# Performance work log

Hardware: AMD Instinct MI355X
Metric: run time of the kernel (lower is better)

## Reference

```python
import jax, jax.numpy as jnp
import numpy as np

RES = 28      # input feature-map resolution
RES2 = 14     # ceil(RES/2) after downsample
NH = 8        # num_heads
KD = 16       # key_dim
D = 64        # attn_ratio * key_dim (per-head value dim)
DH = 512      # D * NH
N = RES * RES
N2 = RES2 * RES2


def _rel_idx():
    # Matches tf.meshgrid default 'xy' indexing in set_attention_bias_idxs.
    r = RES
    kp = np.stack(np.meshgrid(np.arange(r), np.arange(r), indexing='xy')).reshape(2, -1)
    qp = np.stack(np.meshgrid(np.arange(0, r, 2), np.arange(0, r, 2), indexing='xy')).reshape(2, -1)
    rel = np.abs(qp[:, :, None] - kp[:, None, :])
    return jnp.asarray(rel[0] * r + rel[1], dtype=jnp.int32)  # [N2, N]

REL_IDX = _rel_idx()


def _dw_stride2(x, w, b):
    # Depthwise 3x3 conv, stride 2, TF 'SAME' padding. w: [3,3,1,C]
    c = x.shape[-1]
    y = jax.lax.conv_general_dilated(
        x, w, window_strides=(2, 2), padding='SAME',
        dimension_numbers=('NHWC', 'HWIO', 'NHWC'), feature_group_count=c)
    return y + b


def setup_inputs() -> dict:
    key = jax.random.key(0)
    ks = jax.random.split(key, 10)
    f = jnp.float32
    C, OUT = 384, 768
    return {
        'x': jax.random.normal(ks[0], (64, RES, RES, C), f),
        'q_local_w': jax.random.normal(ks[1], (3, 3, 1, C), f) * 0.1,
        'q_local_b': jnp.zeros((C,), f),
        'q_proj_w': jax.random.normal(ks[2], (C, NH * KD), f) * 0.05,
        'q_proj_b': jnp.zeros((NH * KD,), f),
        'q_bn_s': jnp.ones((NH * KD,), f),
        'q_bn_b': jnp.zeros((NH * KD,), f),
        'k_w': jax.random.normal(ks[3], (C, NH * KD), f) * 0.05,
        'k_b': jnp.zeros((NH * KD,), f),
        'k_bn_s': jnp.ones((NH * KD,), f),
        'k_bn_b': jnp.zeros((NH * KD,), f),
        'v_w': jax.random.normal(ks[4], (C, DH), f) * 0.05,
        'v_b': jnp.zeros((DH,), f),
        'v_bn_s': jnp.ones((DH,), f),
        'v_bn_b': jnp.zeros((DH,), f),
        'vloc_w': jax.random.normal(ks[5], (3, 3, 1, DH), f) * 0.1,
        'vloc_b': jnp.zeros((DH,), f),
        'vloc_bn_s': jnp.ones((DH,), f),
        'vloc_bn_b': jnp.zeros((DH,), f),
        'proj_w': jax.random.normal(ks[6], (DH, OUT), f) * 0.05,
        'proj_b': jnp.zeros((OUT,), f),
        'proj_bn_s': jnp.ones((OUT,), f),
        'proj_bn_b': jnp.zeros((OUT,), f),
        'attn_bias': jax.random.normal(ks[7], (NH, N), f) * 0.1,
    }


def reference(x, q_local_w, q_local_b, q_proj_w, q_proj_b, q_bn_s, q_bn_b,
              k_w, k_b, k_bn_s, k_bn_b, v_w, v_b, v_bn_s, v_bn_b,
              vloc_w, vloc_b, vloc_bn_s, vloc_bn_b,
              proj_w, proj_b, proj_bn_s, proj_bn_b, attn_bias):
    B = x.shape[0]
    scale = KD ** -0.5
    # LGQuery: depthwise-conv local branch + 1x1 avg-pool (stride-2 subsample)
    q = _dw_stride2(x, q_local_w, q_local_b) + x[:, ::2, ::2, :]
    q = (q @ q_proj_w + q_proj_b) * q_bn_s + q_bn_b          # [B,14,14,128]
    k = (x @ k_w + k_b) * k_bn_s + k_bn_b                    # [B,28,28,128]
    v = (x @ v_w + v_b) * v_bn_s + v_bn_b                    # [B,28,28,512]
    v_local = _dw_stride2(v, vloc_w, vloc_b) * vloc_bn_s + vloc_bn_b  # [B,14,14,512]
    qh = q.reshape(B, N2, NH, KD).transpose(0, 2, 1, 3)      # [B,H,N2,KD]
    kh = k.reshape(B, N, NH, KD).transpose(0, 2, 3, 1)       # [B,H,KD,N]
    vh = v.reshape(B, N, NH, D).transpose(0, 2, 1, 3)        # [B,H,N,D]
    attn = (qh @ kh) * scale + attn_bias[:, REL_IDX]         # [B,H,N2,N]
    attn = jax.nn.softmax(attn, axis=-1)
    out = (attn @ vh).transpose(0, 2, 1, 3).reshape(B, RES2, RES2, DH)
    out = out + v_local
    # proj: Activation(None) is identity -> 1x1 conv + BN(inference)
    return (out @ proj_w + proj_b) * proj_bn_s + proj_bn_b   # [B,14,14,768]
```

## Files before the change

kernel.cpp:

```cpp
#include <hip/hip_runtime.h>
#include <cstdint>

#define RES    28
#define RES2   14
#define NHEAD  8
#define KDIM   16
#define DV     64
#define DHID   512
#define NSEQ   784
#define N2SEQ  196
#define BATCH  64
#define CIN    384

typedef unsigned short u16;
typedef short  short8_t __attribute__((ext_vector_type(8)));
typedef float  f32x4  __attribute__((ext_vector_type(4)));
typedef u16    us4    __attribute__((ext_vector_type(4)));
typedef u16    us8    __attribute__((ext_vector_type(8)));

__device__ __forceinline__ u16 f2bf(float f) {
    uint32_t u = __float_as_uint(f);
    return (u16)((u + 0x7fffu + ((u >> 16) & 1u)) >> 16);
}
__device__ __forceinline__ float bf2f(u16 h) {
    return __uint_as_float(((uint32_t)h) << 16);
}

__global__ __launch_bounds__(256)
void cast_bf16_kernel(const float* __restrict__ in, u16* __restrict__ out, int n4)
{
    int i = blockIdx.x * 256 + threadIdx.x;
    if (i >= n4) return;
    float4 v = ((const float4*)in)[i];
    us4 r;
    r.x = f2bf(v.x); r.y = f2bf(v.y); r.z = f2bf(v.z); r.w = f2bf(v.w);
    ((us4*)out)[i] = r;
}

__global__ __launch_bounds__(256)
void castT_kernel(const float* __restrict__ W, u16* __restrict__ Wt, int K, int N)
{
    int i = blockIdx.x * 256 + threadIdx.x;
    if (i >= K * N) return;
    int n = i / K, k = i % K;
    Wt[i] = f2bf(W[(size_t)k * N + n]);
}

__global__ void scale_qsb_kernel(const float* __restrict__ s, const float* __restrict__ b,
                                 float* __restrict__ o)
{
    int i = threadIdx.x;
    o[i] = 0.25f * s[i];
    o[128 + i] = 0.25f * b[i];
}

__global__ __launch_bounds__(256)
void biasC_kernel(const float* __restrict__ bias, float* __restrict__ biasC)
{
    int tid = blockIdx.x * 256 + threadIdx.x;
    if (tid >= NHEAD * 13 * 4 * 13 * 64) return;
    int lane = tid & 63;
    int rem  = tid >> 6;
    int qt = rem % 13; rem /= 13;
    int ks = rem % 4;  rem /= 4;
    int ti = rem % 13;
    int h  = rem / 13;
    int col = lane & 15, quad = lane >> 4;
    int q = qt * 16 + col;
    float4 out;
    float* po = &out.x;
    #pragma unroll
    for (int r = 0; r < 4; ++r) {
        int key = ti * 64 + ks * 16 + quad * 4 + r;
        float v;
        if (key >= NSEQ || q >= N2SEQ) {
            v = -1e30f;
        } else {
            int pi = q / 14, pj = q % 14;
            int ku = key / 28, kw = key % 28;
            int d0 = 2 * pj - kw; if (d0 < 0) d0 = -d0;
            int d1 = 2 * pi - ku; if (d1 < 0) d1 = -d1;
            v = bias[h * NSEQ + d0 * 28 + d1];
        }
        po[r] = v;
    }
    ((float4*)biasC)[tid] = out;
}

#define TM 128
#define TN 128
#define TK 32

template<int OUT_MODE>
__global__ __launch_bounds__(256)
void gemm_mfma_kernel(const u16* __restrict__ A, const u16* __restrict__ Bt,
                      const float* __restrict__ bias, const float* __restrict__ scale,
                      const float* __restrict__ shift, void* __restrict__ outp,
                      int M, int N, int K, int rpb)
{
    __shared__ u16 As[TM * TK];
    __shared__ u16 Bs[TN * TK];

    const int t  = threadIdx.x;
    const int w  = t >> 6;
    const int li = t & 63;
    const int wm = w >> 1, wn = w & 1;
    const int bm = blockIdx.x * TM;
    const int bn = blockIdx.y * TN;
    const int m16 = li & 15;
    const int kg  = li >> 4;

    f32x4 acc[4][4];
    #pragma unroll
    for (int i = 0; i < 4; ++i)
        #pragma unroll
        for (int j = 0; j < 4; ++j) acc[i][j] = (f32x4)0.0f;

    for (int k0 = 0; k0 < K; k0 += TK) {
        #pragma unroll
        for (int i = 0; i < 2; ++i) {
            int c   = (w * 2 + i) * 64 + li;
            int row = c >> 2, kc = c & 3;
            const u16* ag = A  + (size_t)(bm + row) * K + k0 + kc * 8;
            const u16* bg = Bt + (size_t)(bn + row) * K + k0 + kc * 8;
            char* la = (char*)As + (size_t)(w * 2 + i) * 64 * 16;
            char* lb = (char*)Bs + (size_t)(w * 2 + i) * 64 * 16;
            __builtin_amdgcn_global_load_lds(
                (const __attribute__((address_space(1))) void*)ag,
                (__attribute__((address_space(3))) void*)la, 16, 0, 0);
            __builtin_amdgcn_global_load_lds(
                (const __attribute__((address_space(1))) void*)bg,
                (__attribute__((address_space(3))) void*)lb, 16, 0, 0);
        }
        __syncthreads();

        short8_t af[4], bf[4];
        #pragma unroll
        for (int mi = 0; mi < 4; ++mi)
            af[mi] = *(const short8_t*)&As[(wm * 64 + mi * 16 + m16) * TK + kg * 8];
        #pragma unroll
        for (int ni = 0; ni < 4; ++ni)
            bf[ni] = *(const short8_t*)&Bs[(wn * 64 + ni * 16 + m16) * TK + kg * 8];

        #pragma unroll
        for (int mi = 0; mi < 4; ++mi)
            #pragma unroll
            for (int ni = 0; ni < 4; ++ni)
                acc[mi][ni] = __builtin_amdgcn_mfma_f32_16x16x32_bf16(
                    af[mi], bf[ni], acc[mi][ni], 0, 0, 0);
        __syncthreads();
    }

    #pragma unroll
    for (int ni = 0; ni < 4; ++ni) {
        const int col = bn + wn * 64 + ni * 16 + m16;
        const float bi = bias[col], sc = scale[col], sh = shift[col];
        #pragma unroll
        for (int mi = 0; mi < 4; ++mi) {
            const int rbase = bm + wm * 64 + mi * 16 + kg * 4;
            #pragma unroll
            for (int r = 0; r < 4; ++r) {
                float val = (acc[mi][ni][r] + bi) * sc + sh;
                const int row = rbase + r;
                if (OUT_MODE == 0) {
                    ((float*)outp)[(size_t)row * N + col] = val;
                } else if (OUT_MODE == 1) {
                    ((u16*)outp)[(size_t)row * N + col] = f2bf(val);
                } else {
                    int bb = row / rpb, tok = row % rpb;
                    int hh = col >> 4;
                    ((u16*)outp)[((size_t)(bb * NHEAD + hh) * rpb + tok) * 16 + (col & 15)] = f2bf(val);
                }
            }
        }
    }
}

__global__ __launch_bounds__(256)
void qin_kernel(const float* __restrict__ x, const float* __restrict__ w,
                const float* __restrict__ b, u16* __restrict__ qin)
{
    const int C4 = CIN / 4;
    int idx = blockIdx.x * 256 + threadIdx.x;
    if (idx >= BATCH * RES2 * RES2 * C4) return;
    int c4 = idx % C4;
    int r  = idx / C4;
    int j  = r % RES2; r /= RES2;
    int i  = r % RES2;
    int bb = r / RES2;

    const float4* x4 = (const float4*)x;
    const float4* w4 = (const float4*)w;
    float4 acc = make_float4(0.f, 0.f, 0.f, 0.f);
    #pragma unroll
    for (int dy = 0; dy < 3; ++dy) {
        int iy = 2 * i + dy;
        if (iy >= RES) continue;
        #pragma unroll
        for (int dx = 0; dx < 3; ++dx) {
            int ix = 2 * j + dx;
            if (ix >= RES) continue;
            float4 xv = x4[((size_t)(bb * RES + iy) * RES + ix) * C4 + c4];
            float4 wv = w4[(dy * 3 + dx) * C4 + c4];
            acc.x += xv.x * wv.x; acc.y += xv.y * wv.y;
            acc.z += xv.z * wv.z; acc.w += xv.w * wv.w;
        }
    }
    float4 bv = ((const float4*)b)[c4];
    float4 xs = x4[((size_t)(bb * RES + 2 * i) * RES + 2 * j) * C4 + c4];
    us4 o;
    o.x = f2bf(acc.x + bv.x + xs.x);
    o.y = f2bf(acc.y + bv.y + xs.y);
    o.z = f2bf(acc.z + bv.z + xs.z);
    o.w = f2bf(acc.w + bv.w + xs.w);
    ((us4*)qin)[idx] = o;
}

__global__ __launch_bounds__(256)
void vloc_kernel(const u16* __restrict__ v, const float* __restrict__ w,
                 const float* __restrict__ b, const float* __restrict__ s,
                 const float* __restrict__ sh, u16* __restrict__ out)
{
    const int C4 = DHID / 4;
    int idx = blockIdx.x * 256 + threadIdx.x;
    if (idx >= BATCH * RES2 * RES2 * C4) return;
    int c4 = idx % C4;
    int r  = idx / C4;
    int j  = r % RES2; r /= RES2;
    int i  = r % RES2;
    int bb = r / RES2;

    const us4* v4 = (const us4*)v;
    const float4* w4 = (const float4*)w;
    float4 acc = make_float4(0.f, 0.f, 0.f, 0.f);
    #pragma unroll
    for (int dy = 0; dy < 3; ++dy) {
        int iy = 2 * i + dy;
        if (iy >= RES) continue;
        #pragma unroll
        for (int dx = 0; dx < 3; ++dx) {
            int ix = 2 * j + dx;
            if (ix >= RES) continue;
            us4 xu = v4[((size_t)(bb * RES + iy) * RES + ix) * C4 + c4];
            float4 wv = w4[(dy * 3 + dx) * C4 + c4];
            acc.x += bf2f(xu.x) * wv.x; acc.y += bf2f(xu.y) * wv.y;
            acc.z += bf2f(xu.z) * wv.z; acc.w += bf2f(xu.w) * wv.w;
        }
    }
    float4 bv = ((const float4*)b)[c4];
    float4 sv = ((const float4*)s)[c4];
    float4 hv = ((const float4*)sh)[c4];
    us4 o;
    o.x = f2bf((acc.x + bv.x) * sv.x + hv.x);
    o.y = f2bf((acc.y + bv.y) * sv.y + hv.y);
    o.z = f2bf((acc.z + bv.z) * sv.z + hv.z);
    o.w = f2bf((acc.w + bv.w) * sv.w + hv.w);
    ((us4*)out)[idx] = o;
}

__global__ __launch_bounds__(256)
void vt_transpose_kernel(const u16* __restrict__ vbuf, u16* __restrict__ vt)
{
    __shared__ u16 tile[64][66];
    const int t  = threadIdx.x;
    const int b  = blockIdx.x;
    const int k0 = blockIdx.y * 64;
    const int h  = blockIdx.z;

    {
        int kr = t >> 2, cc = (t & 3) * 16;
        int key = k0 + kr;
        if (key < NSEQ) {
            const u16* src = vbuf + ((size_t)b * NSEQ + key) * DHID + h * 64 + cc;
            us8 v0 = *(const us8*)src;
            us8 v1 = *(const us8*)(src + 8);
            #pragma unroll
            for (int i = 0; i < 8; ++i) { tile[kr][cc + i] = v0[i]; tile[kr][cc + 8 + i] = v1[i]; }
        }
    }
    __syncthreads();
    {
        int cr = t >> 2, kc = (t & 3) * 16;
        if (k0 + kc < NSEQ) {
            us8 o0, o1;
            #pragma unroll
            for (int i = 0; i < 8; ++i) { o0[i] = tile[kc + i][cr]; o1[i] = tile[kc + 8 + i][cr]; }
            u16* dst = vt + (((size_t)b * NHEAD + h) * 64 + cr) * NSEQ + k0 + kc;
            *(us8*)dst = o0;
            *(us8*)(dst + 8) = o1;
        }
    }
}

__global__ __launch_bounds__(256, 2)
void attn_mfma_kernel(const u16* __restrict__ q, const u16* __restrict__ k,
                      const u16* __restrict__ vt, const float* __restrict__ biasC,
                      u16* __restrict__ io)
{
    __shared__ u16 Ks[64 * 16];
    __shared__ u16 Vs[64 * 68];

    const int t    = threadIdx.x;
    const int w    = t >> 6;
    const int lane = t & 63;
    const int col  = lane & 15;
    const int quad = lane >> 4;
    const int h  = blockIdx.x >> 6;
    const int b  = blockIdx.x & 63;
    const int bh = b * NHEAD + h;

    short8_t qf[4];
    #pragma unroll
    for (int i = 0; i < 4; ++i) {
        int qt = w + 4 * i;
        qf[i] = (short8_t)0;
        if (qt < 13 && quad < 2) {
            int qq = qt * 16 + col; if (qq > 195) qq = 195;
            qf[i] = *(const short8_t*)(q + ((size_t)bh * N2SEQ + qq) * 16 + quad * 8);
        }
    }

    f32x4 O[4][4];
    float m[4], l[4];
    #pragma unroll
    for (int i = 0; i < 4; ++i) {
        m[i] = -3e38f; l[i] = 0.f;
        #pragma unroll
        for (int ns = 0; ns < 4; ++ns) O[i][ns] = (f32x4)0.0f;
    }

    const u16* vtb = vt + (size_t)bh * 64 * NSEQ;
    const u16* kb  = k + (size_t)bh * NSEQ * 16;

    for (int ti = 0; ti < 13; ++ti) {
        const int t0 = ti * 64;
        if (w < 2) {
            int c = w * 64 + lane;
            int tok = t0 + (c >> 1); if (tok > 783) tok = 783;
            const u16* src = kb + (size_t)tok * 16 + (c & 1) * 8;
            char* dst = (char*)Ks + w * 1024;
            __builtin_amdgcn_global_load_lds(
                (const __attribute__((address_space(1))) void*)src,
                (__attribute__((address_space(3))) void*)dst, 16, 0, 0);
        }
        {
            int d = t >> 2, part = t & 3;
            const u16* src = vtb + (size_t)d * NSEQ;
            u16* dst = Vs + d * 68 + part * 16;
            int kk = t0 + part * 16;
            int k0a = kk     > 776 ? 776 : kk;
            int k1a = kk + 8 > 776 ? 776 : kk + 8;
            us8 v0 = *(const us8*)(src + k0a);
            us8 v1 = *(const us8*)(src + k1a);
            us4 a, bb2, c2, d2;
            a.x = v0[0]; a.y = v0[1]; a.z = v0[2]; a.w = v0[3];
            bb2.x = v0[4]; bb2.y = v0[5]; bb2.z = v0[6]; bb2.w = v0[7];
            c2.x = v1[0]; c2.y = v1[1]; c2.z = v1[2]; c2.w = v1[3];
            d2.x = v1[4]; d2.y = v1[5]; d2.z = v1[6]; d2.w = v1[7];
            *(us4*)(dst)      = a;
            *(us4*)(dst + 4)  = bb2;
            *(us4*)(dst + 8)  = c2;
            *(us4*)(dst + 12) = d2;
        }
        __syncthreads();

        short8_t kf[4];
        #pragma unroll
        for (int ks = 0; ks < 4; ++ks) {
            kf[ks] = (short8_t)0;
            if (quad < 2)
                kf[ks] = *(const short8_t*)&Ks[(ks * 16 + col) * 16 + quad * 8];
        }
        short8_t vf[4][2];
        #pragma unroll
        for (int ns = 0; ns < 4; ++ns)
            #pragma unroll
            for (int pr = 0; pr < 2; ++pr) {
                const u16* vrow = &Vs[(ns * 16 + col) * 68 + pr * 32 + quad * 4];
                us4 v0 = *(const us4*)vrow;
                us4 v1 = *(const us4*)(vrow + 16);
                short8_t vv;
                vv[0] = (short)v0.x; vv[1] = (short)v0.y; vv[2] = (short)v0.z; vv[3] = (short)v0.w;
                vv[4] = (short)v1.x; vv[5] = (short)v1.y; vv[6] = (short)v1.z; vv[7] = (short)v1.w;
                vf[ns][pr] = vv;
            }

        #pragma unroll
        for (int i = 0; i < 4; ++i) {
            int qt = w + 4 * i;
            if (qt < 13) {
                f32x4 S[4];
                #pragma unroll
                for (int ks = 0; ks < 4; ++ks) {
                    f32x4 c = *(const f32x4*)(biasC +
                        ((((size_t)h * 13 + ti) * 4 + ks) * 13 + qt) * 256 + lane * 4);
                    S[ks] = __builtin_amdgcn_mfma_f32_16x16x32_bf16(kf[ks], qf[i], c, 0, 0, 0);
                }
                float p[16];
                float mt = -3e38f;
                #pragma unroll
                for (int ks = 0; ks < 4; ++ks)
                    #pragma unroll
                    for (int r = 0; r < 4; ++r) {
                        float lg = S[ks][r];
                        p[ks * 4 + r] = lg;
                        mt = fmaxf(mt, lg);
                    }
                mt = fmaxf(mt, __shfl_xor(mt, 16));
                mt = fmaxf(mt, __shfl_xor(mt, 32));
                float mnew = fmaxf(m[i], mt);
                float alpha = __expf(m[i] - mnew);
                m[i] = mnew;
                float s = 0.f;
                #pragma unroll
                for (int j = 0; j < 16; ++j) { p[j] = __expf(p[j] - mnew); s += p[j]; }
                s += __shfl_xor(s, 16);
                s += __shfl_xor(s, 32);
                l[i] = l[i] * alpha + s;

                float ar[4];
                #pragma unroll
                for (int r = 0; r < 4; ++r) ar[r] = __shfl(alpha, quad * 4 + r);
                #pragma unroll
                for (int ns = 0; ns < 4; ++ns)
                    #pragma unroll
                    for (int r = 0; r < 4; ++r) O[i][ns][r] *= ar[r];

                short8_t pf[2];
                #pragma unroll
                for (int pr = 0; pr < 2; ++pr)
                    #pragma unroll
                    for (int j = 0; j < 8; ++j)
                        pf[pr][j] = (short)f2bf(p[(2 * pr + (j >> 2)) * 4 + (j & 3)]);

                #pragma unroll
                for (int ns = 0; ns < 4; ++ns)
                    #pragma unroll
                    for (int pr = 0; pr < 2; ++pr)
                        O[i][ns] = __builtin_amdgcn_mfma_f32_16x16x32_bf16(
                            pf[pr], vf[ns][pr], O[i][ns], 0, 0, 0);
            }
        }
        __syncthreads();
    }

    #pragma unroll
    for (int i = 0; i < 4; ++i) {
        int qt = w + 4 * i;
        if (qt < 13) {
            float linv = 1.0f / l[i];
            float lr[4];
            #pragma unroll
            for (int r = 0; r < 4; ++r) lr[r] = __shfl(linv, quad * 4 + r);
            #pragma unroll
            for (int ns = 0; ns < 4; ++ns)
                #pragma unroll
                for (int r = 0; r < 4; ++r) {
                    int q2 = qt * 16 + quad * 4 + r;
                    if (q2 < N2SEQ) {
                        size_t a = ((size_t)(b * N2SEQ + q2) * DHID) + h * 64 + ns * 16 + col;
                        io[a] = f2bf(O[i][ns][r] * lr[r] + bf2f(io[a]));
                    }
                }
        }
    }
}

extern "C" void kernel_launch(void* const* d_in, const int* in_sizes, int n_in,
                              void* d_out, int out_size, void* d_ws, size_t ws_size,
                              hipStream_t stream)
{
    const float* x          = (const float*)d_in[0];
    const float* q_local_w  = (const float*)d_in[1];
    const float* q_local_b  = (const float*)d_in[2];
    const float* q_proj_w   = (const float*)d_in[3];
    const float* q_proj_b   = (const float*)d_in[4];
    const float* q_bn_s     = (const float*)d_in[5];
    const float* q_bn_b     = (const float*)d_in[6];
    const float* k_w        = (const float*)d_in[7];
    const float* k_b        = (const float*)d_in[8];
    const float* k_bn_s     = (const float*)d_in[9];
    const float* k_bn_b     = (const float*)d_in[10];
    const float* v_w        = (const float*)d_in[11];
    const float* v_b        = (const float*)d_in[12];
    const float* v_bn_s     = (const float*)d_in[13];
    const float* v_bn_b     = (const float*)d_in[14];
    const float* vloc_w     = (const float*)d_in[15];
    const float* vloc_b     = (const float*)d_in[16];
    const float* vloc_bn_s  = (const float*)d_in[17];
    const float* vloc_bn_b  = (const float*)d_in[18];
    const float* proj_w     = (const float*)d_in[19];
    const float* proj_b     = (const float*)d_in[20];
    const float* proj_bn_s  = (const float*)d_in[21];
    const float* proj_bn_b  = (const float*)d_in[22];
    const float* attn_bias  = (const float*)d_in[23];
    float* out = (float*)d_out;

    const int M1 = BATCH * NSEQ;
    const int M2 = BATCH * N2SEQ;

    char* p = (char*)d_ws;
    u16* xb     = (u16*)p;
    u16* qin_bf = (u16*)(p + 38535168);
    u16* vt     = (u16*)p;
    size_t off = 51380224;
    u16* kwt = (u16*)(p + off);
    u16* vwt = kwt + (size_t)CIN * 128;
    u16* qwt = vwt + (size_t)CIN * DHID;
    u16* pwt = qwt + (size_t)CIN * 128;
    off += 1376256;
    u16* kbuf = (u16*)(p + off);    off += (size_t)M1 * 128 * 2;
    u16* vbuf = (u16*)(p + off);    off += (size_t)M1 * DHID * 2;
    u16* qbuf = (u16*)(p + off);    off += (size_t)M2 * 128 * 2;
    u16* vloc_bf = (u16*)(p + off); off += (size_t)M2 * DHID * 2;
    float* biasC = (float*)(p + off); off += (size_t)NHEAD * 13 * 4 * 13 * 256 * 4;
    float* qsb  = (float*)(p + off);

    {
        int n4 = M1 * CIN / 4;
        cast_bf16_kernel<<<dim3((n4 + 255) / 256), 256, 0, stream>>>(x, xb, n4);
    }
    castT_kernel<<<dim3((CIN * 128 + 255) / 256), 256, 0, stream>>>(k_w, kwt, CIN, 128);
    castT_kernel<<<dim3((CIN * DHID + 255) / 256), 256, 0, stream>>>(v_w, vwt, CIN, DHID);
    castT_kernel<<<dim3((CIN * 128 + 255) / 256), 256, 0, stream>>>(q_proj_w, qwt, CIN, 128);
    castT_kernel<<<dim3((DHID * 768 + 255) / 256), 256, 0, stream>>>(proj_w, pwt, DHID, 768);
    scale_qsb_kernel<<<dim3(1), 128, 0, stream>>>(q_bn_s, q_bn_b, qsb);
    {
        int items = NHEAD * 13 * 4 * 13 * 64;
        biasC_kernel<<<dim3((items + 255) / 256), 256, 0, stream>>>(attn_bias, biasC);
    }
    {
        int items = M2 * (CIN / 4);
        qin_kernel<<<dim3((items + 255) / 256), 256, 0, stream>>>(x, q_local_w, q_local_b, qin_bf);
    }
    gemm_mfma_kernel<2><<<dim3(M1 / TM, 128 / TN), 256, 0, stream>>>(
        xb, kwt, k_b, k_bn_s, k_bn_b, kbuf, M1, 128, CIN, NSEQ);
    gemm_mfma_kernel<1><<<dim3(M1 / TM, DHID / TN), 256, 0, stream>>>(
        xb, vwt, v_b, v_bn_s, v_bn_b, vbuf, M1, DHID, CIN, 0);
    gemm_mfma_kernel<2><<<dim3(M2 / TM, 128 / TN), 256, 0, stream>>>(
        qin_bf, qwt, q_proj_b, qsb, qsb + 128, qbuf, M2, 128, CIN, N2SEQ);

    vt_transpose_kernel<<<dim3(BATCH, 13, NHEAD), 256, 0, stream>>>(vbuf, vt);

    {
        int items = M2 * (DHID / 4);
        vloc_kernel<<<dim3((items + 255) / 256), 256, 0, stream>>>(
            vbuf, vloc_w, vloc_b, vloc_bn_s, vloc_bn_b, vloc_bf);
    }
    attn_mfma_kernel<<<dim3(NHEAD * BATCH), 256, 0, stream>>>(
        qbuf, kbuf, vt, biasC, vloc_bf);

    gemm_mfma_kernel<0><<<dim3(M2 / TM, 768 / TN), 256, 0, stream>>>(
        vloc_bf, pwt, proj_b, proj_bn_s, proj_bn_b, out, M2, 768, DHID, 0);
}
```

Measured before the change: 423.1 us.

## Fuse x cast into K/V GEMM, merge prep kernels, split attention blocks

Drops the separate fp32-to-bf16 cast of x: the GEMM now loads fp32 A tiles and converts them into LDS itself. The K and V projections become one GEMM with N=640 whose epilogue writes to two buffers. Weight transposes and bias/scale setup are merged into a single prep kernel. Attention launches twice as many blocks, each covering half the query tiles, to raise occupancy. These changes cut launches and one full read and write of x, at the cost of synchronous fp32 loads replacing the async global-to-LDS path for A.

Measured after the change: 416.3 us. About the same (-1.6%).

```diff
diff --git a/kernel.cpp b/kernel.cpp
--- a/kernel.cpp
+++ b/kernel.cpp
@@ -26,32 +26,53 @@
     return __uint_as_float(((uint32_t)h) << 16);
 }
 
+#define PREP_N (49152 + 196608 + 49152 + 393216 + 1920 + 256)
 __global__ __launch_bounds__(256)
-void cast_bf16_kernel(const float* __restrict__ in, u16* __restrict__ out, int n4)
+void prep_kernel(const float* __restrict__ k_w, const float* __restrict__ v_w,
+                 const float* __restrict__ q_proj_w, const float* __restrict__ proj_w,
+                 const float* __restrict__ k_b, const float* __restrict__ v_b,
+                 const float* __restrict__ k_bn_s, const float* __restrict__ v_bn_s,
+                 const float* __restrict__ k_bn_b, const float* __restrict__ v_bn_b,
+                 const float* __restrict__ q_bn_s, const float* __restrict__ q_bn_b,
+                 u16* __restrict__ kvwt, u16* __restrict__ qwt, u16* __restrict__ pwt,
+                 float* __restrict__ kv_eps, float* __restrict__ qsb)
 {
     int i = blockIdx.x * 256 + threadIdx.x;
-    if (i >= n4) return;
-    float4 v = ((const float4*)in)[i];
-    us4 r;
-    r.x = f2bf(v.x); r.y = f2bf(v.y); r.z = f2bf(v.z); r.w = f2bf(v.w);
-    ((us4*)out)[i] = r;
-}
-
-__global__ __launch_bounds__(256)
-void castT_kernel(const float* __restrict__ W, u16* __restrict__ Wt, int K, int N)
-{
-    int i = blockIdx.x * 256 + threadIdx.x;
-    if (i >= K * N) return;
-    int n = i / K, k = i % K;
-    Wt[i] = f2bf(W[(size_t)k * N + n]);
-}
-
-__global__ void scale_qsb_kernel(const float* __restrict__ s, const float* __restrict__ b,
-                                 float* __restrict__ o)
-{
-    int i = threadIdx.x;
-    o[i] = 0.25f * s[i];
-    o[128 + i] = 0.25f * b[i];
+    if (i >= PREP_N) return;
+    if (i < 49152) {
+        int n = i / 384, k = i % 384;
+        kvwt[i] = f2bf(k_w[(size_t)k * 128 + n]);
+        return;
+    }
+    i -= 49152;
+    if (i < 196608) {
+        int n = i / 384, k = i % 384;
+        kvwt[49152 + i] = f2bf(v_w[(size_t)k * 512 + n]);
+        return;
+    }
+    i -= 196608;
+    if (i < 49152) {
+        int n = i / 384, k = i % 384;
+        qwt[i] = f2bf(q_proj_w[(size_t)k * 128 + n]);
+        return;
+    }
+    i -= 49152;
+    if (i < 393216) {
+        int n = i / 512, k = i % 512;
+        pwt[i] = f2bf(proj_w[(size_t)k * 768 + n]);
+        return;
+    }
+    i -= 393216;
+    if (i < 1920) {
+        int which = i / 640, j = i % 640;
+        const float* a = which == 0 ? (j < 128 ? k_b : v_b)
+                       : which == 1 ? (j < 128 ? k_bn_s : v_bn_s)
+                                    : (j < 128 ? k_bn_b : v_bn_b);
+        kv_eps[i] = a[j < 128 ? j : j - 128];
+        return;
+    }
+    i -= 1920;
+    qsb[i] = 0.25f * (i < 128 ? q_bn_s[i] : q_bn_b[i - 128]);
 }
 
 __global__ __launch_bounds__(256)
@@ -91,12 +112,12 @@
 #define TN 128
 #define TK 32
 
-template<int OUT_MODE>
+template<int OUT_MODE, int A_FP32>
 __global__ __launch_bounds__(256)
-void gemm_mfma_kernel(const u16* __restrict__ A, const u16* __restrict__ Bt,
+void gemm_mfma_kernel(const void* __restrict__ Av, const u16* __restrict__ Bt,
                       const float* __restrict__ bias, const float* __restrict__ scale,
                       const float* __restrict__ shift, void* __restrict__ outp,
-                      int M, int N, int K, int rpb)
+                      u16* __restrict__ out2, int M, int N, int K, int rpb)
 {
     __shared__ u16 As[TM * TK];
     __shared__ u16 Bs[TN * TK];
@@ -121,13 +142,23 @@
         for (int i = 0; i < 2; ++i) {
             int c   = (w * 2 + i) * 64 + li;
             int row = c >> 2, kc = c & 3;
-            const u16* ag = A  + (size_t)(bm + row) * K + k0 + kc * 8;
+            if (A_FP32) {
+                const float* ag = (const float*)Av + (size_t)(bm + row) * K + k0 + kc * 8;
+                float4 a0 = *(const float4*)ag;
+                float4 a1 = *(const float4*)(ag + 4);
+                us8 vv;
+                vv[0] = f2bf(a0.x); vv[1] = f2bf(a0.y); vv[2] = f2bf(a0.z); vv[3] = f2bf(a0.w);
+                vv[4] = f2bf(a1.x); vv[5] = f2bf(a1.y); vv[6] = f2bf(a1.z); vv[7] = f2bf(a1.w);
+                *(us8*)&As[(size_t)row * TK + kc * 8] = vv;
+            } else {
+                const u16* ag = (const u16*)Av + (size_t)(bm + row) * K + k0 + kc * 8;
+                char* la = (char*)As + (size_t)(w * 2 + i) * 64 * 16;
+                __builtin_amdgcn_global_load_lds(
+                    (const __attribute__((address_space(1))) void*)ag,
+                    (__attribute__((address_space(3))) void*)la, 16, 0, 0);
+            }
             const u16* bg = Bt + (size_t)(bn + row) * K + k0 + kc * 8;
-            char* la = (char*)As + (size_t)(w * 2 + i) * 64 * 16;
             char* lb = (char*)Bs + (size_t)(w * 2 + i) * 64 * 16;
-            __builtin_amdgcn_global_load_lds(
-                (const __attribute__((address_space(1))) void*)ag,
-                (__attribute__((address_space(3))) void*)la, 16, 0, 0);
             __builtin_amdgcn_global_load_lds(
                 (const __attribute__((address_space(1))) void*)bg,
                 (__attribute__((address_space(3))) void*)lb, 16, 0, 0);
@@ -166,10 +197,18 @@
                     ((float*)outp)[(size_t)row * N + col] = val;
                 } else if (OUT_MODE == 1) {
                     ((u16*)outp)[(size_t)row * N + col] = f2bf(val);
-                } else {
+                } else if (OUT_MODE == 2) {
                     int bb = row / rpb, tok = row % rpb;
                     int hh = col >> 4;
                     ((u16*)outp)[((size_t)(bb * NHEAD + hh) * rpb + tok) * 16 + (col & 15)] = f2bf(val);
+                } else {
+                    if (bn < 128) {
+                        int bb = row / NSEQ, tok = row % NSEQ;
+                        int hh = col >> 4;
+                        ((u16*)outp)[((size_t)(bb * NHEAD + hh) * NSEQ + tok) * 16 + (col & 15)] = f2bf(val);
+                    } else {
+                        out2[(size_t)row * DHID + (col - 128)] = f2bf(val);
+                    }
                 }
             }
         }
@@ -305,14 +344,16 @@
     const int lane = t & 63;
     const int col  = lane & 15;
     const int quad = lane >> 4;
-    const int h  = blockIdx.x >> 6;
-    const int b  = blockIdx.x & 63;
+    const int par = blockIdx.x & 1;
+    const int bhx = blockIdx.x >> 1;
+    const int h  = bhx >> 6;
+    const int b  = bhx & 63;
     const int bh = b * NHEAD + h;
 
-    short8_t qf[4];
-    #pragma unroll
-    for (int i = 0; i < 4; ++i) {
-        int qt = w + 4 * i;
+    short8_t qf[2];
+    #pragma unroll
+    for (int i = 0; i < 2; ++i) {
+        int qt = w + 4 * (par * 2 + i);
         qf[i] = (short8_t)0;
         if (qt < 13 && quad < 2) {
             int qq = qt * 16 + col; if (qq > 195) qq = 195;
@@ -320,10 +361,10 @@
         }
     }
 
-    f32x4 O[4][4];
-    float m[4], l[4];
-    #pragma unroll
-    for (int i = 0; i < 4; ++i) {
+    f32x4 O[2][4];
+    float m[2], l[2];
+    #pragma unroll
+    for (int i = 0; i < 2; ++i) {
         m[i] = -3e38f; l[i] = 0.f;
         #pragma unroll
         for (int ns = 0; ns < 4; ++ns) O[i][ns] = (f32x4)0.0f;
@@ -386,8 +427,8 @@
             }
 
         #pragma unroll
-        for (int i = 0; i < 4; ++i) {
-            int qt = w + 4 * i;
+        for (int i = 0; i < 2; ++i) {
+            int qt = w + 4 * (par * 2 + i);
             if (qt < 13) {
                 f32x4 S[4];
                 #pragma unroll
@@ -445,8 +486,8 @@
     }
 
     #pragma unroll
-    for (int i = 0; i < 4; ++i) {
-        int qt = w + 4 * i;
+    for (int i = 0; i < 2; ++i) {
+        int qt = w + 4 * (par * 2 + i);
         if (qt < 13) {
             float linv = 1.0f / l[i];
             float lr[4];
@@ -500,31 +541,23 @@
     const int M2 = BATCH * N2SEQ;
 
     char* p = (char*)d_ws;
-    u16* xb     = (u16*)p;
-    u16* qin_bf = (u16*)(p + 38535168);
+    u16* qin_bf = (u16*)p;
     u16* vt     = (u16*)p;
     size_t off = 51380224;
-    u16* kwt = (u16*)(p + off);
-    u16* vwt = kwt + (size_t)CIN * 128;
-    u16* qwt = vwt + (size_t)CIN * DHID;
-    u16* pwt = qwt + (size_t)CIN * 128;
-    off += 1376256;
+    u16* kvwt = (u16*)(p + off);  off += 640 * 384 * 2;
+    u16* qwt  = (u16*)(p + off);  off += 128 * 384 * 2;
+    u16* pwt  = (u16*)(p + off);  off += 768 * 512 * 2;
+    float* kv_eps = (float*)(p + off); off += 1920 * 4;
+    float* qsb    = (float*)(p + off); off += 256 * 4;
     u16* kbuf = (u16*)(p + off);    off += (size_t)M1 * 128 * 2;
     u16* vbuf = (u16*)(p + off);    off += (size_t)M1 * DHID * 2;
     u16* qbuf = (u16*)(p + off);    off += (size_t)M2 * 128 * 2;
     u16* vloc_bf = (u16*)(p + off); off += (size_t)M2 * DHID * 2;
-    float* biasC = (float*)(p + off); off += (size_t)NHEAD * 13 * 4 * 13 * 256 * 4;
-    float* qsb  = (float*)(p + off);
-
-    {
-        int n4 = M1 * CIN / 4;
-        cast_bf16_kernel<<<dim3((n4 + 255) / 256), 256, 0, stream>>>(x, xb, n4);
-    }
-    castT_kernel<<<dim3((CIN * 128 + 255) / 256), 256, 0, stream>>>(k_w, kwt, CIN, 128);
-    castT_kernel<<<dim3((CIN * DHID + 255) / 256), 256, 0, stream>>>(v_w, vwt, CIN, DHID);
-    castT_kernel<<<dim3((CIN * 128 + 255) / 256), 256, 0, stream>>>(q_proj_w, qwt, CIN, 128);
-    castT_kernel<<<dim3((DHID * 768 + 255) / 256), 256, 0, stream>>>(proj_w, pwt, DHID, 768);
-    scale_qsb_kernel<<<dim3(1), 128, 0, stream>>>(q_bn_s, q_bn_b, qsb);
+    float* biasC = (float*)(p + off);
+
+    prep_kernel<<<dim3((PREP_N + 255) / 256), 256, 0, stream>>>(
+        k_w, v_w, q_proj_w, proj_w, k_b, v_b, k_bn_s, v_bn_s, k_bn_b, v_bn_b,
+        q_bn_s, q_bn_b, kvwt, qwt, pwt, kv_eps, qsb);
     {
         int items = NHEAD * 13 * 4 * 13 * 64;
         biasC_kernel<<<dim3((items + 255) / 256), 256, 0, stream>>>(attn_bias, biasC);
@@ -533,12 +566,10 @@
         int items = M2 * (CIN / 4);
         qin_kernel<<<dim3((items + 255) / 256), 256, 0, stream>>>(x, q_local_w, q_local_b, qin_bf);
     }
-    gemm_mfma_kernel<2><<<dim3(M1 / TM, 128 / TN), 256, 0, stream>>>(
-        xb, kwt, k_b, k_bn_s, k_bn_b, kbuf, M1, 128, CIN, NSEQ);
-    gemm_mfma_kernel<1><<<dim3(M1 / TM, DHID / TN), 256, 0, stream>>>(
-        xb, vwt, v_b, v_bn_s, v_bn_b, vbuf, M1, DHID, CIN, 0);
-    gemm_mfma_kernel<2><<<dim3(M2 / TM, 128 / TN), 256, 0, stream>>>(
-        qin_bf, qwt, q_proj_b, qsb, qsb + 128, qbuf, M2, 128, CIN, N2SEQ);
+    gemm_mfma_kernel<3, 1><<<dim3(M1 / TM, 640 / TN), 256, 0, stream>>>(
+        x, kvwt, kv_eps, kv_eps + 640, kv_eps + 1280, kbuf, vbuf, M1, 640, CIN, NSEQ);
+    gemm_mfma_kernel<2, 0><<<dim3(M2 / TM, 128 / TN), 256, 0, stream>>>(
+        qin_bf, qwt, q_proj_b, qsb, qsb + 128, qbuf, nullptr, M2, 128, CIN, N2SEQ);
 
     vt_transpose_kernel<<<dim3(BATCH, 13, NHEAD), 256, 0, stream>>>(vbuf, vt);
 
@@ -547,9 +578,9 @@
         vloc_kernel<<<dim3((items + 255) / 256), 256, 0, stream>>>(
             vbuf, vloc_w, vloc_b, vloc_bn_s, vloc_bn_b, vloc_bf);
     }
-    attn_mfma_kernel<<<dim3(NHEAD * BATCH), 256, 0, stream>>>(
+    attn_mfma_kernel<<<dim3(NHEAD * BATCH * 2), 256, 0, stream>>>(
         qbuf, kbuf, vt, biasC, vloc_bf);
 
-    gemm_mfma_kernel<0><<<dim3(M2 / TM, 768 / TN), 256, 0, stream>>>(
-        vloc_bf, pwt, proj_b, proj_bn_s, proj_bn_b, out, M2, 768, DHID, 0);
-}
+    gemm_mfma_kernel<0, 0><<<dim3(M2 / TM, 768 / TN), 256, 0, stream>>>(
+        vloc_bf, pwt, proj_b, proj_bn_s, proj_bn_b, out, nullptr, M2, 768, DHID, 0);
+}
```
